# Kernel optimization log

Hardware: AMD Instinct MI355X
Metric: run time of the kernel (lower is better)

Reference implementation:

```python
import jax, jax.numpy as jnp
import numpy as np

WS = 16
NB = 800
THRESH = 0.05


def setup_inputs() -> dict:
    key = jax.random.key(0)
    k1, k2, k3, k4 = jax.random.split(key, 4)
    tensor_msi = jax.random.uniform(k1, (1, 64, 512, 512), dtype=jnp.float32)
    tensor_he = jax.random.uniform(k2, (1, 3, 512, 512), dtype=jnp.float32)
    i_idx = jax.random.randint(k3, (NB,), 0, 512 - WS, dtype=jnp.int32)
    j_idx = jax.random.randint(k4, (NB,), 0, 512 - WS, dtype=jnp.int32)
    return {
        "tensor_msi": tensor_msi,
        "tensor_he": tensor_he,
        "i_idx": i_idx,
        "j_idx": j_idx,
        "window_size": WS,
        "batch": NB,
    }


def reference(tensor_msi, tensor_he, i_idx, j_idx, window_size, batch):
    u = tensor_msi.shape[1]
    msi = tensor_msi[:, : u // 2]  # only first half of MSI channels is used
    ws = window_size
    p = ws * ws

    def get_patch(x, i, j):
        # x: [1, C, M, N] -> [C, ws*ws]
        c = x.shape[1]
        patch = jax.lax.dynamic_slice(x, (0, 0, i, j), (1, c, ws, ws))
        return patch.reshape(c, p)

    def pdist2(x, mask):
        # pairwise squared L2 distance over positions: D[a,b] = sum_k (x[k,a]-x[k,b])^2
        sq = jnp.sum(x * x, axis=0)  # [p]
        gram = jnp.einsum("kp,kq->pq", x, x)  # [p, p]
        d = sq[:, None] + sq[None, :] - 2.0 * gram
        # zero out rows/cols where the HE patch intensity sum < THRESH
        return d * mask[:, None] * mask[None, :]

    def per_patch(i, j):
        pm = get_patch(msi, i, j)  # [u//2, p]
        ph = get_patch(tensor_he, i, j)  # [3, p]
        # NOTE: original code computes index_zero from MSI then overwrites it
        # with the HE-based one; only the HE mask is applied to both.
        mask = (jnp.sum(ph, axis=0) >= THRESH).astype(pm.dtype)  # [p]
        dm = pdist2(pm, mask)
        dh = jax.lax.stop_gradient(pdist2(ph, mask))  # .detach()
        return jnp.mean(jnp.abs(dm - dh))  # L1Loss mean

    losses = jax.vmap(per_patch)(i_idx, j_idx)  # [batch]
    return jnp.sum(losses) / (batch // 5)
```

## Files before the change

### kernel.cpp

```cpp
#include <hip/hip_runtime.h>
#include <hip/hip_bf16.h>


#define PSZ  256
#define IMG  512
#define IMG2 (IMG * IMG)
#define XSTR 40

typedef __attribute__((ext_vector_type(8))) short short8;
typedef __attribute__((ext_vector_type(4))) float float4v;

static __device__ __forceinline__ unsigned short f2bf(float v) {
    union { __hip_bfloat16 b; unsigned short u; } cv;
    cv.b = __float2bfloat16(v);
    return cv.u;
}
static __device__ __forceinline__ float bf2f(unsigned short u) {
    union { unsigned int u; float f; } cv;
    cv.u = ((unsigned int)u) << 16;
    return cv.f;
}

__global__ __launch_bounds__(256, 4)
void corr_loss_kernel(const float* __restrict__ msi,
                      const float* __restrict__ he,
                      const int* __restrict__ i_idx,
                      const int* __restrict__ j_idx,
                      float* __restrict__ partial)
{
    __shared__ __align__(16) unsigned short xs[PSZ * XSTR];
    __shared__ __align__(16) unsigned short eA[PSZ * 8];
    __shared__ __align__(16) unsigned short eB[PSZ * 8];
    __shared__ float red[4];

    const int b = blockIdx.x;
    const int t = threadIdx.x;
    const int i0 = i_idx[b], j0 = j_idx[b];

    {
        const int r = t >> 4, c = t & 15;
        const float* hp = he + (size_t)(i0 + r) * IMG + (j0 + c);
        const float* mp = msi + (size_t)(i0 + r) * IMG + (j0 + c);

        float h0 = hp[0], h1 = hp[IMG2], h2 = hp[2 * IMG2];
        float v[32];
#pragma unroll
        for (int ch = 0; ch < 32; ++ch) v[ch] = mp[(size_t)ch * IMG2];

        const float mf = (h0 + h1 + h2 >= 0.05f) ? 1.f : 0.f;
        const unsigned short hb0 = f2bf(h0 * mf), hb1 = f2bf(h1 * mf), hb2 = f2bf(h2 * mf);
        const float hr0 = bf2f(hb0), hr1 = bf2f(hb1), hr2 = bf2f(hb2);
        const float sh = hr0 * hr0 + hr1 * hr1 + hr2 * hr2;

        float sm = 0.f;
#pragma unroll
        for (int g = 0; g < 4; ++g) {
            unsigned int pk[4];
#pragma unroll
            for (int k = 0; k < 4; ++k) {
                unsigned short lo = f2bf(v[g * 8 + 2 * k]     * mf);
                unsigned short hi = f2bf(v[g * 8 + 2 * k + 1] * mf);
                float fl = bf2f(lo), fh = bf2f(hi);
                sm = fmaf(fl, fl, sm);
                sm = fmaf(fh, fh, sm);
                pk[k] = (unsigned int)lo | ((unsigned int)hi << 16);
            }
            *(uint4*)&xs[t * XSTR + g * 8] = make_uint4(pk[0], pk[1], pk[2], pk[3]);
        }
        const float s = sm - sh;
        const unsigned short shi = f2bf(s);
        const unsigned short slo = f2bf(s - bf2f(shi));
        const unsigned short mb  = (mf != 0.f) ? (unsigned short)0x3F80 : (unsigned short)0;
        const unsigned short d0  = f2bf(2.f * hr0);
        const unsigned short d1  = f2bf(2.f * hr1);
        const unsigned short d2  = f2bf(2.f * hr2);
        *(uint4*)&eA[t * 8] = make_uint4(
            (unsigned)d0 | ((unsigned)d1 << 16),
            (unsigned)d2 | ((unsigned)shi << 16),
            (unsigned)slo | ((unsigned)mb << 16),
            (unsigned)mb);
        *(uint4*)&eB[t * 8] = make_uint4(
            (unsigned)hb0 | ((unsigned)hb1 << 16),
            (unsigned)hb2 | ((unsigned)mb << 16),
            (unsigned)mb | ((unsigned)shi << 16),
            (unsigned)slo);
    }
    __syncthreads();

    const int lane = t & 63, w = t >> 6;
    const int mrow = lane & 15, quad = lane >> 4;
    const short8 zfrag = {0, 0, 0, 0, 0, 0, 0, 0};

    short8 Am[4], Ah[4];
#pragma unroll
    for (int ii = 0; ii < 4; ++ii) {
        const int ri = ((w << 2) + ii) * 16 + mrow;
        uint4 u = *(const uint4*)&xs[ri * XSTR + (quad << 3)];
        u.x = (u.x ^ 0x80008000u) + 0x00800080u;
        u.y = (u.y ^ 0x80008000u) + 0x00800080u;
        u.z = (u.z ^ 0x80008000u) + 0x00800080u;
        u.w = (u.w ^ 0x80008000u) + 0x00800080u;
        Am[ii] = *(const short8*)&u;
        Ah[ii] = (quad == 0) ? *(const short8*)&eA[ri << 3] : zfrag;
    }

    float acc[4] = {0.f, 0.f, 0.f, 0.f};
#pragma unroll 4
    for (int j = 0; j < 16; ++j) {
        const int cj = (j << 4) + mrow;
        short8 Bm = *(const short8*)&xs[cj * XSTR + (quad << 3)];
        short8 Bh = (quad == 0) ? *(const short8*)&eB[cj << 3] : zfrag;
        float4v g[4];
#pragma unroll
        for (int ii = 0; ii < 4; ++ii) {
            g[ii] = (float4v){0.f, 0.f, 0.f, 0.f};
            g[ii] = __builtin_amdgcn_mfma_f32_16x16x32_bf16(Ah[ii], Bh, g[ii], 0, 0, 0);
            g[ii] = __builtin_amdgcn_mfma_f32_16x16x32_bf16(Am[ii], Bm, g[ii], 0, 0, 0);
        }
#pragma unroll
        for (int ii = 0; ii < 4; ++ii) {
            acc[ii] += fabsf(g[ii][0]);
            acc[ii] += fabsf(g[ii][1]);
            acc[ii] += fabsf(g[ii][2]);
            acc[ii] += fabsf(g[ii][3]);
        }
    }
    float a = (acc[0] + acc[1]) + (acc[2] + acc[3]);

#pragma unroll
    for (int off = 32; off > 0; off >>= 1)
        a += __shfl_down(a, off, 64);
    if (lane == 0) red[w] = a;
    __syncthreads();
    if (t == 0)
        partial[b] = (red[0] + red[1]) + (red[2] + red[3]);
}

__global__ __launch_bounds__(256)
void reduce_kernel(const float* __restrict__ partial, float* __restrict__ out,
                   int n, float scale)
{
    __shared__ float red[4];
    float a = 0.f;
    for (int i = threadIdx.x; i < n; i += 256) a += partial[i];
#pragma unroll
    for (int off = 32; off > 0; off >>= 1)
        a += __shfl_down(a, off, 64);
    const int lane = threadIdx.x & 63, w = threadIdx.x >> 6;
    if (lane == 0) red[w] = a;
    __syncthreads();
    if (threadIdx.x == 0)
        out[0] = ((red[0] + red[1]) + (red[2] + red[3])) * scale;
}

extern "C" void kernel_launch(void* const* d_in, const int* in_sizes, int n_in,
                              void* d_out, int out_size, void* d_ws, size_t ws_size,
                              hipStream_t stream) {
    const float* msi   = (const float*)d_in[0];
    const float* he    = (const float*)d_in[1];
    const int*   i_idx = (const int*)d_in[2];
    const int*   j_idx = (const int*)d_in[3];
    const int    NB    = in_sizes[2];
    float*       out   = (float*)d_out;
    float*       part  = (float*)d_ws;

    const float scale = 1.0f / ((float)(PSZ * PSZ) * (float)(NB / 5));
    corr_loss_kernel<<<NB, 256, 0, stream>>>(msi, he, i_idx, j_idx, part);
    reduce_kernel<<<1, 256, 0, stream>>>(part, out, NB, scale);
}
```

Before: 108.7 us.

## Precompute per-pixel packed bf16 records in a full-image prep pass

Adds a prep kernel that turns every image pixel into a 112-byte bf16 record. Each record holds the 32 masked MSI channels, the HE terms, the squared-norm hi/lo split and the mask values. The patch kernel then does six contiguous 16-byte loads per pixel instead of 35 strided fp32 channel loads plus conversion math. In exchange the whole 512x512 image is processed and about 29MB of records are written, even though patches cover only part of it. The layout also assumes the workspace is larger than 32MB.

```diff
diff --git a/kernel.cpp b/kernel.cpp
--- a/kernel.cpp
+++ b/kernel.cpp
@@ -5,7 +5,7 @@
 #define PSZ  256
 #define IMG  512
 #define IMG2 (IMG * IMG)
-#define XSTR 40
+#define REC  56
 
 typedef __attribute__((ext_vector_type(8))) short short8;
 typedef __attribute__((ext_vector_type(4))) float float4v;
@@ -22,15 +22,65 @@
 }
 
 __global__ __launch_bounds__(256, 4)
-void corr_loss_kernel(const float* __restrict__ msi,
-                      const float* __restrict__ he,
+void prep_kernel(const float* __restrict__ msi,
+                 const float* __restrict__ he,
+                 unsigned short* __restrict__ rec)
+{
+    const int idx = blockIdx.x * 256 + threadIdx.x;
+
+    const float h0 = he[idx], h1 = he[IMG2 + idx], h2 = he[2 * IMG2 + idx];
+    float v[32];
+#pragma unroll
+    for (int ch = 0; ch < 32; ++ch) v[ch] = msi[(size_t)ch * IMG2 + idx];
+
+    const float mf = (h0 + h1 + h2 >= 0.05f) ? 1.f : 0.f;
+    const unsigned short hb0 = f2bf(h0 * mf), hb1 = f2bf(h1 * mf), hb2 = f2bf(h2 * mf);
+    const float hr0 = bf2f(hb0), hr1 = bf2f(hb1), hr2 = bf2f(hb2);
+    const float sh = hr0 * hr0 + hr1 * hr1 + hr2 * hr2;
+
+    float sm = 0.f;
+    unsigned int pk[16];
+#pragma unroll
+    for (int k = 0; k < 16; ++k) {
+        unsigned short lo = f2bf(v[2 * k]     * mf);
+        unsigned short hi = f2bf(v[2 * k + 1] * mf);
+        float fl = bf2f(lo), fh = bf2f(hi);
+        sm = fmaf(fl, fl, sm);
+        sm = fmaf(fh, fh, sm);
+        pk[k] = (unsigned int)lo | ((unsigned int)hi << 16);
+    }
+    const float s = sm - sh;
+    const unsigned short shi = f2bf(s);
+    const unsigned short slo = f2bf(s - bf2f(shi));
+    const unsigned short mb  = (mf != 0.f) ? (unsigned short)0x3F80 : (unsigned short)0;
+    const unsigned short d0  = f2bf(2.f * hr0);
+    const unsigned short d1  = f2bf(2.f * hr1);
+    const unsigned short d2  = f2bf(2.f * hr2);
+
+    unsigned short* rp = rec + (size_t)idx * REC;
+#pragma unroll
+    for (int k = 0; k < 4; ++k)
+        *(uint4*)(rp + k * 8) = make_uint4(pk[4 * k], pk[4 * k + 1],
+                                           pk[4 * k + 2], pk[4 * k + 3]);
+    *(uint4*)(rp + 32) = make_uint4(
+        (unsigned)d0 | ((unsigned)d1 << 16),
+        (unsigned)d2 | ((unsigned)shi << 16),
+        (unsigned)slo | ((unsigned)mb << 16),
+        (unsigned)mb);
+    *(uint4*)(rp + 40) = make_uint4(
+        (unsigned)hb0 | ((unsigned)hb1 << 16),
+        (unsigned)hb2 | ((unsigned)mb << 16),
+        (unsigned)mb | ((unsigned)shi << 16),
+        (unsigned)slo);
+}
+
+__global__ __launch_bounds__(256, 4)
+void corr_loss_kernel(const unsigned short* __restrict__ rec,
                       const int* __restrict__ i_idx,
                       const int* __restrict__ j_idx,
                       float* __restrict__ partial)
 {
-    __shared__ __align__(16) unsigned short xs[PSZ * XSTR];
-    __shared__ __align__(16) unsigned short eA[PSZ * 8];
-    __shared__ __align__(16) unsigned short eB[PSZ * 8];
+    __shared__ __align__(16) unsigned short xs[PSZ * REC];
     __shared__ float red[4];
 
     const int b = blockIdx.x;
@@ -39,51 +89,13 @@
 
     {
         const int r = t >> 4, c = t & 15;
-        const float* hp = he + (size_t)(i0 + r) * IMG + (j0 + c);
-        const float* mp = msi + (size_t)(i0 + r) * IMG + (j0 + c);
-
-        float h0 = hp[0], h1 = hp[IMG2], h2 = hp[2 * IMG2];
-        float v[32];
+        const unsigned short* gp =
+            rec + (size_t)((i0 + r) * IMG + (j0 + c)) * REC;
+        uint4 u[6];
 #pragma unroll
-        for (int ch = 0; ch < 32; ++ch) v[ch] = mp[(size_t)ch * IMG2];
-
-        const float mf = (h0 + h1 + h2 >= 0.05f) ? 1.f : 0.f;
-        const unsigned short hb0 = f2bf(h0 * mf), hb1 = f2bf(h1 * mf), hb2 = f2bf(h2 * mf);
-        const float hr0 = bf2f(hb0), hr1 = bf2f(hb1), hr2 = bf2f(hb2);
-        const float sh = hr0 * hr0 + hr1 * hr1 + hr2 * hr2;
-
-        float sm = 0.f;
+        for (int k = 0; k < 6; ++k) u[k] = *(const uint4*)(gp + k * 8);
 #pragma unroll
-        for (int g = 0; g < 4; ++g) {
-            unsigned int pk[4];
-#pragma unroll
-            for (int k = 0; k < 4; ++k) {
-                unsigned short lo = f2bf(v[g * 8 + 2 * k]     * mf);
-                unsigned short hi = f2bf(v[g * 8 + 2 * k + 1] * mf);
-                float fl = bf2f(lo), fh = bf2f(hi);
-                sm = fmaf(fl, fl, sm);
-                sm = fmaf(fh, fh, sm);
-                pk[k] = (unsigned int)lo | ((unsigned int)hi << 16);
-            }
-            *(uint4*)&xs[t * XSTR + g * 8] = make_uint4(pk[0], pk[1], pk[2], pk[3]);
-        }
-        const float s = sm - sh;
-        const unsigned short shi = f2bf(s);
-        const unsigned short slo = f2bf(s - bf2f(shi));
-        const unsigned short mb  = (mf != 0.f) ? (unsigned short)0x3F80 : (unsigned short)0;
-        const unsigned short d0  = f2bf(2.f * hr0);
-        const unsigned short d1  = f2bf(2.f * hr1);
-        const unsigned short d2  = f2bf(2.f * hr2);
-        *(uint4*)&eA[t * 8] = make_uint4(
-            (unsigned)d0 | ((unsigned)d1 << 16),
-            (unsigned)d2 | ((unsigned)shi << 16),
-            (unsigned)slo | ((unsigned)mb << 16),
-            (unsigned)mb);
-        *(uint4*)&eB[t * 8] = make_uint4(
-            (unsigned)hb0 | ((unsigned)hb1 << 16),
-            (unsigned)hb2 | ((unsigned)mb << 16),
-            (unsigned)mb | ((unsigned)shi << 16),
-            (unsigned)slo);
+        for (int k = 0; k < 6; ++k) *(uint4*)&xs[t * REC + k * 8] = u[k];
     }
     __syncthreads();
 
@@ -95,21 +107,21 @@
 #pragma unroll
     for (int ii = 0; ii < 4; ++ii) {
         const int ri = ((w << 2) + ii) * 16 + mrow;
-        uint4 u = *(const uint4*)&xs[ri * XSTR + (quad << 3)];
+        uint4 u = *(const uint4*)&xs[ri * REC + (quad << 3)];
         u.x = (u.x ^ 0x80008000u) + 0x00800080u;
         u.y = (u.y ^ 0x80008000u) + 0x00800080u;
         u.z = (u.z ^ 0x80008000u) + 0x00800080u;
         u.w = (u.w ^ 0x80008000u) + 0x00800080u;
         Am[ii] = *(const short8*)&u;
-        Ah[ii] = (quad == 0) ? *(const short8*)&eA[ri << 3] : zfrag;
+        Ah[ii] = (quad == 0) ? *(const short8*)&xs[ri * REC + 32] : zfrag;
     }
 
     float acc[4] = {0.f, 0.f, 0.f, 0.f};
 #pragma unroll 4
     for (int j = 0; j < 16; ++j) {
         const int cj = (j << 4) + mrow;
-        short8 Bm = *(const short8*)&xs[cj * XSTR + (quad << 3)];
-        short8 Bh = (quad == 0) ? *(const short8*)&eB[cj << 3] : zfrag;
+        short8 Bm = *(const short8*)&xs[cj * REC + (quad << 3)];
+        short8 Bh = (quad == 0) ? *(const short8*)&xs[cj * REC + 40] : zfrag;
         float4v g[4];
 #pragma unroll
         for (int ii = 0; ii < 4; ++ii) {
@@ -162,9 +174,12 @@
     const int*   j_idx = (const int*)d_in[3];
     const int    NB    = in_sizes[2];
     float*       out   = (float*)d_out;
-    float*       part  = (float*)d_ws;
+
+    unsigned short* rec  = (unsigned short*)d_ws;
+    float*          part = (float*)((char*)d_ws + (32u << 20));
 
     const float scale = 1.0f / ((float)(PSZ * PSZ) * (float)(NB / 5));
-    corr_loss_kernel<<<NB, 256, 0, stream>>>(msi, he, i_idx, j_idx, part);
+    prep_kernel<<<IMG2 / 256, 256, 0, stream>>>(msi, he, rec);
+    corr_loss_kernel<<<NB, 256, 0, stream>>>(rec, i_idx, j_idx, part);
     reduce_kernel<<<1, 256, 0, stream>>>(part, out, NB, scale);
 }
```

After: 123.3 us. 13.4% more time.
